# Optimization experiments

Measured on AMD Instinct MI355X. Metric: run time of the kernel, lower is better.

## Reference

```python
import jax, jax.numpy as jnp
import numpy as np

THR = 0.2        # config['thr']
BORDER_RM = 2    # config['border_rm']


def _border_valid(h, w, b):
    # Flattened [h*w] bool mask: True for cells at least b away from every border.
    r = jnp.arange(h)
    c = jnp.arange(w)
    vr = (r >= b) & (r < h - b)
    vc = (c >= b) & (c < w - b)
    return (vr[:, None] & vc[None, :]).reshape(-1)


def setup_inputs() -> dict:
    key = jax.random.key(0)
    h0c, w0c, h1c, w1c = 60, 80, 60, 80   # coarse grid (640x480 / 8)
    N = 4
    conf = jax.random.uniform(key, (N, h0c * w0c, h1c * w1c), dtype=jnp.float32)
    return {"conf_matrix": conf, "h0c": h0c, "w0c": w0c, "h1c": h1c, "w1c": w1c}


def reference(conf_matrix, h0c, w0c, h1c, w1c):
    # conf_matrix: [N, L, S], L = h0c*w0c, S = h1c*w1c
    valid0 = _border_valid(h0c, w0c, BORDER_RM)   # [L]
    valid1 = _border_valid(h1c, w1c, BORDER_RM)   # [S]

    # threshold + border removal (equivalent to mask_border on the 5D view)
    mask = (conf_matrix > THR) & valid0[None, :, None] & valid1[None, None, :]

    # mutual nearest neighbor: keep only entries that are both row-max and col-max
    rowmax = jnp.max(conf_matrix, axis=2, keepdims=True)   # [N, L, 1]
    colmax = jnp.max(conf_matrix, axis=1, keepdims=True)   # [N, 1, S]
    mask = mask & (conf_matrix == rowmax) & (conf_matrix == colmax)

    # torch's mask.max(dim=2) on bool -> (any, first-True index)
    all_j_ids = jnp.argmax(mask, axis=2)                   # [N, L] int
    mask_v = jnp.any(mask, axis=2)                         # [N, L] bool
    mconf = jnp.take_along_axis(conf_matrix, all_j_ids[:, :, None], axis=2)[:, :, 0]
    mconf = mconf * mask_v                                 # zero where no match
    return mconf, mask_v, all_j_ids
```

## Files before the change

### kernel.cpp

```cpp
#include <hip/hip_runtime.h>
#include <cfloat>

#define THRV 0.2f
#define H0 60
#define W0 80
#define H1 60
#define W1 80
#define LL (H0 * W0)
#define SS (H1 * W1)
#define BR 2

__global__ void __launch_bounds__(256) colmax_kernel(
    const float* __restrict__ conf, unsigned int* __restrict__ colmax,
    int rowsPerBlock) {
  int s = blockIdx.x * 256 + threadIdx.x;
  if (s >= SS) return;
  int n = blockIdx.z;
  int l0 = blockIdx.y * rowsPerBlock;
  int l1 = min(l0 + rowsPerBlock, LL);
  const float* p = conf + ((size_t)n * LL + l0) * SS + s;
  float m = 0.0f;
  for (int l = l0; l < l1; ++l) {
    m = fmaxf(m, *p);
    p += SS;
  }
  atomicMax(&colmax[n * SS + s], __float_as_uint(m));
}

__global__ void __launch_bounds__(256) row_kernel(
    const float* __restrict__ conf, const unsigned int* __restrict__ colmax,
    float* __restrict__ out, int N) {
  int l = blockIdx.x;
  int n = blockIdx.y;
  int tid = threadIdx.x;
  const int NL = N * LL;

  int r0 = l / W0, c0 = l % W0;
  bool valid0 = (r0 >= BR) && (r0 < H0 - BR) && (c0 >= BR) && (c0 < W0 - BR);
  if (!valid0) {
    if (tid == 0) {
      out[n * LL + l] = 0.0f;
      out[NL + n * LL + l] = 0.0f;
      out[2 * NL + n * LL + l] = 0.0f;
    }
    return;
  }

  __shared__ float row[SS];
  __shared__ float wmax[4];
  __shared__ int s_minidx;

  const float* p = conf + ((size_t)n * LL + l) * SS;
  float m = -FLT_MAX;
  for (int s = tid; s < SS; s += 256) {
    float v = p[s];
    row[s] = v;
    m = fmaxf(m, v);
  }
  for (int off = 32; off > 0; off >>= 1) m = fmaxf(m, __shfl_down(m, off, 64));
  if ((tid & 63) == 0) wmax[tid >> 6] = m;
  if (tid == 0) s_minidx = 0x7fffffff;
  __syncthreads();
  float rowmax = fmaxf(fmaxf(wmax[0], wmax[1]), fmaxf(wmax[2], wmax[3]));

  if (rowmax > THRV) {
    const unsigned int* cm = colmax + n * SS;
    for (int s = tid; s < SS; s += 256) {
      float v = row[s];
      if (v == rowmax) {
        int r1 = s / W1, c1 = s % W1;
        bool valid1 = (r1 >= BR) && (r1 < H1 - BR) && (c1 >= BR) && (c1 < W1 - BR);
        if (valid1 && v == __uint_as_float(cm[s])) atomicMin(&s_minidx, s);
      }
    }
  }
  __syncthreads();

  if (tid == 0) {
    int j = s_minidx;
    bool found = (j != 0x7fffffff);
    out[n * LL + l] = found ? rowmax : 0.0f;
    out[NL + n * LL + l] = found ? 1.0f : 0.0f;
    out[2 * NL + n * LL + l] = found ? (float)j : 0.0f;
  }
}

extern "C" void kernel_launch(void* const* d_in, const int* in_sizes, int n_in,
                              void* d_out, int out_size, void* d_ws, size_t ws_size,
                              hipStream_t stream) {
  const float* conf = (const float*)d_in[0];
  int N = in_sizes[0] / (LL * SS);
  float* out = (float*)d_out;
  unsigned int* colmax = (unsigned int*)d_ws;

  hipMemsetAsync(colmax, 0, (size_t)N * SS * sizeof(unsigned int), stream);

  const int L_CHUNKS = 25;
  dim3 g1((SS + 255) / 256, L_CHUNKS, N);
  colmax_kernel<<<g1, 256, 0, stream>>>(conf, colmax, (LL + L_CHUNKS - 1) / L_CHUNKS);

  dim3 g2(LL, N);
  row_kernel<<<g2, 256, 0, stream>>>(conf, colmax, out, N);
}
```

Measured before the change: 624.5 us.

## Fuse column-max and row-max scans into one pass with candidate lists

Replaces the two full passes over the confidence matrix (column-max, then row-max plus match) with a single fused scan. Each block processes 12 rows, accumulates per-thread column maxima in registers, and records up to 8 row-max candidate positions per row. A small resolve kernel then checks those candidates against the global column max, falling back to a serial row rescan if there are too many. This roughly halves HBM traffic over the 368MB input, at the cost of extra workspace and a slow serial fallback path.

Measured after the change: 594.5 us. -4.8%, faster.

```diff
diff --git a/kernel.cpp b/kernel.cpp
--- a/kernel.cpp
+++ b/kernel.cpp
@@ -9,96 +9,156 @@
 #define LL (H0 * W0)
 #define SS (H1 * W1)
 #define BR 2
+#define KCAND 8
+#define RPB 12
 
-__global__ void __launch_bounds__(256) colmax_kernel(
-    const float* __restrict__ conf, unsigned int* __restrict__ colmax,
-    int rowsPerBlock) {
-  int s = blockIdx.x * 256 + threadIdx.x;
-  if (s >= SS) return;
-  int n = blockIdx.z;
-  int l0 = blockIdx.y * rowsPerBlock;
-  int l1 = min(l0 + rowsPerBlock, LL);
-  const float* p = conf + ((size_t)n * LL + l0) * SS + s;
-  float m = 0.0f;
-  for (int l = l0; l < l1; ++l) {
-    m = fmaxf(m, *p);
-    p += SS;
+__global__ void __launch_bounds__(256) fused_scan(
+    const float* __restrict__ conf,
+    unsigned int* __restrict__ colmax,
+    float* __restrict__ rowmaxArr,
+    int* __restrict__ candCnt,
+    int* __restrict__ candPos)
+{
+  const int tid = threadIdx.x;
+  const int n = blockIdx.y;
+  const int l0 = blockIdx.x * RPB;
+
+  __shared__ float wred[4];
+  __shared__ int lcnt;
+  __shared__ int lpos[KCAND];
+  if (tid == 0) lcnt = 0;
+
+  float4 cm[5];
+#pragma unroll
+  for (int k = 0; k < 5; ++k) cm[k] = make_float4(0.f, 0.f, 0.f, 0.f);
+  __syncthreads();
+
+  for (int r = 0; r < RPB; ++r) {
+    const int l = l0 + r;
+    const float4* rowp = (const float4*)(conf + ((size_t)n * LL + l) * SS);
+
+    float4 d[5];
+    float tm = -1.f;
+#pragma unroll
+    for (int k = 0; k < 5; ++k) {
+      const int i = tid + 256 * k;
+      if (i < 1200) {
+        float4 v = rowp[i];
+        d[k] = v;
+        cm[k].x = fmaxf(cm[k].x, v.x);
+        cm[k].y = fmaxf(cm[k].y, v.y);
+        cm[k].z = fmaxf(cm[k].z, v.z);
+        cm[k].w = fmaxf(cm[k].w, v.w);
+        tm = fmaxf(tm, fmaxf(fmaxf(v.x, v.y), fmaxf(v.z, v.w)));
+      } else {
+        d[k] = make_float4(-1.f, -1.f, -1.f, -1.f);
+      }
+    }
+
+#pragma unroll
+    for (int off = 32; off; off >>= 1) tm = fmaxf(tm, __shfl_xor(tm, off, 64));
+    if ((tid & 63) == 0) wred[tid >> 6] = tm;
+    __syncthreads();
+    const float rowmax = fmaxf(fmaxf(wred[0], wred[1]), fmaxf(wred[2], wred[3]));
+
+    const int r0 = l / W0, c0 = l % W0;
+    const bool valid0 = (r0 >= BR) && (r0 < H0 - BR) && (c0 >= BR) && (c0 < W0 - BR);
+
+    if (valid0 && rowmax > THRV) {
+#pragma unroll
+      for (int k = 0; k < 5; ++k) {
+        const int i = tid + 256 * k;
+        const float4 v = d[k];
+        if (v.x == rowmax) { int ix = atomicAdd(&lcnt, 1); if (ix < KCAND) lpos[ix] = 4 * i + 0; }
+        if (v.y == rowmax) { int ix = atomicAdd(&lcnt, 1); if (ix < KCAND) lpos[ix] = 4 * i + 1; }
+        if (v.z == rowmax) { int ix = atomicAdd(&lcnt, 1); if (ix < KCAND) lpos[ix] = 4 * i + 2; }
+        if (v.w == rowmax) { int ix = atomicAdd(&lcnt, 1); if (ix < KCAND) lpos[ix] = 4 * i + 3; }
+      }
+    }
+    __syncthreads();
+
+    const int row = n * LL + l;
+    const int c = lcnt;
+    if (tid == 0) { candCnt[row] = c; rowmaxArr[row] = rowmax; }
+    if (tid < (c < KCAND ? c : KCAND)) candPos[row * KCAND + tid] = lpos[tid];
+    __syncthreads();
+    if (tid == 0) lcnt = 0;
   }
-  atomicMax(&colmax[n * SS + s], __float_as_uint(m));
+
+#pragma unroll
+  for (int k = 0; k < 5; ++k) {
+    const int i = tid + 256 * k;
+    if (i < 1200) {
+      unsigned int* base = colmax + n * SS + 4 * i;
+      atomicMax(base + 0, __float_as_uint(cm[k].x));
+      atomicMax(base + 1, __float_as_uint(cm[k].y));
+      atomicMax(base + 2, __float_as_uint(cm[k].z));
+      atomicMax(base + 3, __float_as_uint(cm[k].w));
+    }
+  }
 }
 
-__global__ void __launch_bounds__(256) row_kernel(
-    const float* __restrict__ conf, const unsigned int* __restrict__ colmax,
-    float* __restrict__ out, int N) {
-  int l = blockIdx.x;
-  int n = blockIdx.y;
-  int tid = threadIdx.x;
+__global__ void __launch_bounds__(256) resolve(
+    const float* __restrict__ conf,
+    const unsigned int* __restrict__ colmax,
+    const float* __restrict__ rowmaxArr,
+    const int* __restrict__ candCnt,
+    const int* __restrict__ candPos,
+    float* __restrict__ out, int N)
+{
+  const int row = blockIdx.x * 256 + threadIdx.x;
   const int NL = N * LL;
+  if (row >= NL) return;
+  const int n = row / LL;
 
-  int r0 = l / W0, c0 = l % W0;
-  bool valid0 = (r0 >= BR) && (r0 < H0 - BR) && (c0 >= BR) && (c0 < W0 - BR);
-  if (!valid0) {
-    if (tid == 0) {
-      out[n * LL + l] = 0.0f;
-      out[NL + n * LL + l] = 0.0f;
-      out[2 * NL + n * LL + l] = 0.0f;
-    }
-    return;
-  }
-
-  __shared__ float row[SS];
-  __shared__ float wmax[4];
-  __shared__ int s_minidx;
-
-  const float* p = conf + ((size_t)n * LL + l) * SS;
-  float m = -FLT_MAX;
-  for (int s = tid; s < SS; s += 256) {
-    float v = p[s];
-    row[s] = v;
-    m = fmaxf(m, v);
-  }
-  for (int off = 32; off > 0; off >>= 1) m = fmaxf(m, __shfl_down(m, off, 64));
-  if ((tid & 63) == 0) wmax[tid >> 6] = m;
-  if (tid == 0) s_minidx = 0x7fffffff;
-  __syncthreads();
-  float rowmax = fmaxf(fmaxf(wmax[0], wmax[1]), fmaxf(wmax[2], wmax[3]));
-
-  if (rowmax > THRV) {
-    const unsigned int* cm = colmax + n * SS;
-    for (int s = tid; s < SS; s += 256) {
-      float v = row[s];
-      if (v == rowmax) {
-        int r1 = s / W1, c1 = s % W1;
-        bool valid1 = (r1 >= BR) && (r1 < H1 - BR) && (c1 >= BR) && (c1 < W1 - BR);
-        if (valid1 && v == __uint_as_float(cm[s])) atomicMin(&s_minidx, s);
+  float mconf = 0.f, mv = 0.f, jid = 0.f;
+  const int c = candCnt[row];
+  if (c > 0) {
+    const float rowmax = rowmaxArr[row];
+    const unsigned int rmu = __float_as_uint(rowmax);
+    const unsigned int* cmn = colmax + n * SS;
+    int best = 0x7fffffff;
+    if (c <= KCAND) {
+      for (int i = 0; i < c; ++i) {
+        const int s = candPos[row * KCAND + i];
+        const int r1 = s / W1, c1 = s % W1;
+        const bool valid1 = (r1 >= BR) && (r1 < H1 - BR) && (c1 >= BR) && (c1 < W1 - BR);
+        if (valid1 && cmn[s] == rmu && s < best) best = s;
+      }
+    } else {
+      const float* rp = conf + (size_t)row * SS;
+      for (int s = 0; s < SS; ++s) {
+        if (rp[s] == rowmax) {
+          const int r1 = s / W1, c1 = s % W1;
+          const bool valid1 = (r1 >= BR) && (r1 < H1 - BR) && (c1 >= BR) && (c1 < W1 - BR);
+          if (valid1 && cmn[s] == rmu) { best = s; break; }
+        }
       }
     }
+    if (best != 0x7fffffff) { mconf = rowmax; mv = 1.f; jid = (float)best; }
   }
-  __syncthreads();
-
-  if (tid == 0) {
-    int j = s_minidx;
-    bool found = (j != 0x7fffffff);
-    out[n * LL + l] = found ? rowmax : 0.0f;
-    out[NL + n * LL + l] = found ? 1.0f : 0.0f;
-    out[2 * NL + n * LL + l] = found ? (float)j : 0.0f;
-  }
+  out[row] = mconf;
+  out[NL + row] = mv;
+  out[2 * NL + row] = jid;
 }
 
 extern "C" void kernel_launch(void* const* d_in, const int* in_sizes, int n_in,
                               void* d_out, int out_size, void* d_ws, size_t ws_size,
                               hipStream_t stream) {
   const float* conf = (const float*)d_in[0];
-  int N = in_sizes[0] / (LL * SS);
+  const int N = in_sizes[0] / (LL * SS);
   float* out = (float*)d_out;
+
   unsigned int* colmax = (unsigned int*)d_ws;
+  float* rowmaxArr = (float*)(colmax + (size_t)N * SS);
+  int* candCnt = (int*)(rowmaxArr + (size_t)N * LL);
+  int* candPos = candCnt + (size_t)N * LL;
 
   hipMemsetAsync(colmax, 0, (size_t)N * SS * sizeof(unsigned int), stream);
 
-  const int L_CHUNKS = 25;
-  dim3 g1((SS + 255) / 256, L_CHUNKS, N);
-  colmax_kernel<<<g1, 256, 0, stream>>>(conf, colmax, (LL + L_CHUNKS - 1) / L_CHUNKS);
+  dim3 g1(LL / RPB, N);
+  fused_scan<<<g1, 256, 0, stream>>>(conf, colmax, rowmaxArr, candCnt, candPos);
 
-  dim3 g2(LL, N);
-  row_kernel<<<g2, 256, 0, stream>>>(conf, colmax, out, N);
+  const int NL = N * LL;
+  resolve<<<(NL + 255) / 256, 256, 0, stream>>>(conf, colmax, rowmaxArr, candCnt, candPos, out, N);
 }
```
